# Kernel optimization log

Measured on AMD Instinct MI355X. Metric: run time of the kernel, lower is better.

## Reference

```python
import jax, jax.numpy as jnp
import numpy as np

KERNEL = 25
PAD = (KERNEL - 1) // 2  # 12
LN_EPS = 1e-5
CAP_FACTOR = 2.0
K_VALUE = 2


def _moving_avg(x):
    # x: [B, L, D]; Autoformer moving_avg: replicate-pad ends, avg-pool k=25 stride 1
    front = jnp.repeat(x[:, :1, :], PAD, axis=1)
    end = jnp.repeat(x[:, -1:, :], PAD, axis=1)
    xp = jnp.concatenate([front, x, end], axis=1)            # [B, L+2*PAD, D]
    cs = jnp.cumsum(xp, axis=1)
    cs = jnp.concatenate([jnp.zeros_like(cs[:, :1]), cs], axis=1)
    return (cs[:, KERNEL:] - cs[:, :-KERNEL]) / KERNEL        # [B, L, D]


def _layernorm(h, g, b):
    mu = jnp.mean(h, axis=-1, keepdims=True)
    d = h - mu
    var = jnp.mean(d * d, axis=-1, keepdims=True)
    return d * jax.lax.rsqrt(var + LN_EPS) * g + b


def setup_inputs() -> dict:
    key = jax.random.key(0)
    ks = jax.random.split(key, 6)
    B, L, D, H, E = 32, 512, 512, 1024, 8
    sd_in = 1.0 / np.sqrt(D)
    sd_h = 1.0 / np.sqrt(H)
    return {
        "x": jax.random.normal(ks[0], (B, L, D), jnp.float32),
        "Wt": jax.random.normal(ks[1], (D, H), jnp.float32) * sd_in,
        "bt": jax.random.normal(ks[2], (H,), jnp.float32) * sd_in,
        "gt": jnp.ones((H,), jnp.float32),
        "bet": jnp.zeros((H,), jnp.float32),
        "Ws": jax.random.normal(ks[3], (D, H), jnp.float32) * sd_in,
        "bs": jax.random.normal(ks[4], (H,), jnp.float32) * sd_in,
        "gs": jnp.ones((H,), jnp.float32),
        "bes": jnp.zeros((H,), jnp.float32),
        "W2": jax.random.normal(ks[5], (H, E), jnp.float32) * sd_h,
        "b2": jnp.zeros((E,), jnp.float32),
    }


def reference(x, Wt, bt, gt, bet, Ws, bs, gs, bes, W2, b2):
    # series decomposition: (residual, moving_mean) -> (trend_init, seasonal_init)
    ma = _moving_avg(x)
    trend_init = x - ma          # residual (first return of series_decomp)
    seasonal_init = ma           # moving mean (second return)

    t = _layernorm(trend_init @ Wt + bt, gt, bet)       # [B, L, H]
    s = _layernorm(seasonal_init @ Ws + bs, gs, bes)    # [B, L, H]
    med = jax.nn.relu(t + s)
    logits = med @ W2 + b2                               # [B, L, E]
    gate_scores = jax.nn.softmax(logits, axis=-1)

    B, L, E = gate_scores.shape
    capacity = int(CAP_FACTOR * B)

    _, top_k_indices = jax.lax.top_k(gate_scores, K_VALUE)  # [B, L, K]
    # torch scatter_(1, idx, 1) on 3D: mask[b, idx[b,l,j], j] = 1
    bi = jnp.arange(B)[:, None, None]
    ji = jnp.arange(K_VALUE)[None, None, :]
    mask = jnp.zeros_like(gate_scores).at[bi, top_k_indices, ji].set(1.0)

    masked = gate_scores * mask
    denom = jnp.sum(masked, axis=0, keepdims=True) + 1e-4    # [1, L, E]
    return masked / denom * capacity
```

## Files before the change

kernel.cpp:

```cpp
#include <hip/hip_runtime.h>

#define NB 32
#define NL 512
#define ND 512
#define NH 1024
#define NE 8
#define NROWS (NB * NL)
#define CW 2048
#define SPAD 136

typedef __attribute__((ext_vector_type(8))) short bf16x8;
typedef __attribute__((ext_vector_type(4))) float f32x4;
typedef __attribute__((ext_vector_type(4))) unsigned u32x4;

__device__ __forceinline__ unsigned short f2bf(float f) {
    unsigned u = __float_as_uint(f);
    return (unsigned short)((u + 0x7fffu + ((u >> 16) & 1u)) >> 16);
}
__device__ __forceinline__ float bf2f(unsigned short b) {
    return __uint_as_float(((unsigned)b) << 16);
}
__device__ __forceinline__ unsigned pktr(float a, float b) {
    return __builtin_amdgcn_perm(__float_as_uint(b), __float_as_uint(a), 0x07060302u);
}

__global__ __launch_bounds__(256) void wprep(
    const float* __restrict__ Wt, const float* __restrict__ Ws,
    unsigned* __restrict__ bpack)
{
    __shared__ float tile[64][65];
    int bid = blockIdx.x;
    int mat = bid >> 7, rem = bid & 127;
    int kt0 = (rem >> 4) << 6;
    int nt0 = (rem & 15) << 6;
    const float* W = mat ? Ws : Wt;
    unsigned* Oh = bpack;
    unsigned* Ol = bpack + 524288u;
    int t = threadIdx.x;
    #pragma unroll
    for (int i = 0; i < 16; ++i) {
        int idx = t + 256 * i;
        int k = idx >> 6, n = idx & 63;
        tile[k][n] = W[(size_t)(kt0 + k) * NH + nt0 + n];
    }
    __syncthreads();
    #pragma unroll
    for (int i = 0; i < 8; ++i) {
        int idx = t + 256 * i;
        int jp = idx & 3, lane = (idx >> 2) & 63, kbr = (idx >> 8) & 1, ntr = (idx >> 9) & 3;
        int ncol = ntr * 16 + (lane & 15);
        int kcol = kbr * 32 + ((lane >> 4) << 3) + jp * 2;
        float w0 = tile[kcol][ncol], w1 = tile[kcol + 1][ncol];
        unsigned short h0 = f2bf(w0), h1 = f2bf(w1);
        unsigned short l0 = f2bf(w0 - bf2f(h0)), l1 = f2bf(w1 - bf2f(h1));
        int ntg = mat * 64 + (nt0 >> 4) + ntr;
        int kb = (kt0 >> 5) + kbr;
        unsigned offs = ((unsigned)(ntg * 16 + kb) * 64u + (unsigned)lane) * 4u + jp;
        Oh[offs] = (unsigned)h0 | ((unsigned)h1 << 16);
        Ol[offs] = (unsigned)l0 | ((unsigned)l1 << 16);
    }
}

__global__ __launch_bounds__(512, 4) void gemm_all(
    const float* __restrict__ x, const unsigned* __restrict__ bpack,
    unsigned short* __restrict__ C, unsigned short* __restrict__ Clo)
{
    __shared__ union {
        unsigned short A[2][128][64];
        unsigned short cs[64][264];
    } sm;

    const int tid = threadIdx.x, lane = tid & 63, wave = tid >> 6;
    const int g = lane >> 4, c = lane & 15;

    if (blockIdx.x >= 256) {
        const int wm = wave >> 2, wn = wave & 3;
        const int bid = blockIdx.x - 256;
        const int xcd = bid & 7, idx = bid >> 3;
        const int mi = xcd * 16 + (idx >> 3), ni = idx & 7;
        const int m0 = mi * 128;

        f32x4 acc[4][4];
        #pragma unroll
        for (int nf = 0; nf < 4; ++nf)
            #pragma unroll
            for (int mf = 0; mf < 4; ++mf) acc[nf][mf] = (f32x4){0.f, 0.f, 0.f, 0.f};

        const int srow = tid >> 2, sj = tid & 3;
        const int wcol = (sj * 8) ^ ((srow & 7) << 3);
        const float* xs = x + (size_t)(m0 + srow) * ND + sj * 8;

        auto loadB = [&](int kb2, int nf) -> bf16x8 {
            int nt = ni * 16 + wn * 4 + nf;
            return *(const bf16x8*)(bpack + ((size_t)(nt * 16 + kb2) * 64 + lane) * 4);
        };

        float4 xa = *(const float4*)xs;
        float4 xb = *(const float4*)(xs + 4);
        bf16x8 bc0 = loadB(0, 0), bc1 = loadB(0, 1), bc2 = loadB(0, 2), bc3 = loadB(0, 3);

        int p = 0;
        for (int kb = 0; kb < 16; ++kb) {
            u32x4 u;
            u.x = pktr(xa.x, xa.y); u.y = pktr(xa.z, xa.w);
            u.z = pktr(xb.x, xb.y); u.w = pktr(xb.z, xb.w);
            *(u32x4*)&sm.A[p][srow][wcol] = u;
            __syncthreads();

            bf16x8 bn0, bn1, bn2, bn3;
            if (kb < 15) {
                const float* pn = xs + (kb + 1) * 32;
                xa = *(const float4*)pn;
                xb = *(const float4*)(pn + 4);
                bn0 = loadB(kb + 1, 0); bn1 = loadB(kb + 1, 1);
                bn2 = loadB(kb + 1, 2); bn3 = loadB(kb + 1, 3);
            }

            bf16x8 af[4];
            #pragma unroll
            for (int mf = 0; mf < 4; ++mf) {
                int R = wm * 64 + mf * 16 + c;
                int rcol = (g * 8) ^ ((R & 7) << 3);
                af[mf] = *(const bf16x8*)&sm.A[p][R][rcol];
            }
            #pragma unroll
            for (int mf = 0; mf < 4; ++mf) {
                acc[0][mf] = __builtin_amdgcn_mfma_f32_16x16x32_bf16(af[mf], bc0, acc[0][mf], 0, 0, 0);
                acc[1][mf] = __builtin_amdgcn_mfma_f32_16x16x32_bf16(af[mf], bc1, acc[1][mf], 0, 0, 0);
                acc[2][mf] = __builtin_amdgcn_mfma_f32_16x16x32_bf16(af[mf], bc2, acc[2][mf], 0, 0, 0);
                acc[3][mf] = __builtin_amdgcn_mfma_f32_16x16x32_bf16(af[mf], bc3, acc[3][mf], 0, 0, 0);
            }
            if (kb < 15) { bc0 = bn0; bc1 = bn1; bc2 = bn2; bc3 = bn3; }
            p ^= 1;
        }

        #pragma unroll
        for (int ph = 0; ph < 2; ++ph) {
            __syncthreads();
            if (wm == ph) {
                #pragma unroll
                for (int nf = 0; nf < 4; ++nf)
                    #pragma unroll
                    for (int mf = 0; mf < 4; ++mf)
                        #pragma unroll
                        for (int r = 0; r < 4; ++r)
                            sm.cs[mf * 16 + g * 4 + r][wn * 64 + nf * 16 + c] =
                                (unsigned short)(__float_as_uint(acc[nf][mf][r]) >> 16);
            }
            __syncthreads();
            int row = tid >> 3, ch = tid & 7;
            int grow = m0 + ph * 64 + row;
            if ((grow & 511) >= 32) {
                unsigned short* dst = &C[(size_t)grow * CW + ni * 256 + ch * 32];
                #pragma unroll
                for (int q = 0; q < 4; ++q)
                    *(uint4*)(dst + q * 8) = *(const uint4*)&sm.cs[row][ch * 32 + q * 8];
            }
        }
    } else {
        const int eb = blockIdx.x;
        const int bq = eb >> 3, ni = eb & 7;
        const int m0 = bq * NL;
        const unsigned* Bhi = bpack;
        const unsigned* Blo = bpack + 524288u;

        f32x4 acc[2][2];
        #pragma unroll
        for (int nf = 0; nf < 2; ++nf)
            #pragma unroll
            for (int mf = 0; mf < 2; ++mf) acc[nf][mf] = (f32x4){0.f, 0.f, 0.f, 0.f};

        const float* xr0 = x + (size_t)(m0 + c) * ND + g * 8;
        #pragma unroll 2
        for (int kb = 0; kb < 16; ++kb) {
            bf16x8 ah[2], al[2];
            #pragma unroll
            for (int mf = 0; mf < 2; ++mf) {
                const float* p = xr0 + mf * (16 * ND) + kb * 32;
                float4 a0 = *(const float4*)p;
                float4 a1 = *(const float4*)(p + 4);
                float f[8] = {a0.x, a0.y, a0.z, a0.w, a1.x, a1.y, a1.z, a1.w};
                float lo[8];
                #pragma unroll
                for (int j = 0; j < 8; ++j) {
                    float hif = __uint_as_float(__float_as_uint(f[j]) & 0xFFFF0000u);
                    lo[j] = f[j] - hif;
                }
                u32x4 uh, ul;
                uh.x = pktr(f[0], f[1]); uh.y = pktr(f[2], f[3]);
                uh.z = pktr(f[4], f[5]); uh.w = pktr(f[6], f[7]);
                ul.x = pktr(lo[0], lo[1]); ul.y = pktr(lo[2], lo[3]);
                ul.z = pktr(lo[4], lo[5]); ul.w = pktr(lo[6], lo[7]);
                ah[mf] = __builtin_bit_cast(bf16x8, uh);
                al[mf] = __builtin_bit_cast(bf16x8, ul);
            }
            #pragma unroll
            for (int nf = 0; nf < 2; ++nf) {
                int nt = ni * 16 + wave * 2 + nf;
                size_t bo = ((size_t)(nt * 16 + kb) * 64 + lane) * 4;
                bf16x8 bh = *(const bf16x8*)(Bhi + bo);
                bf16x8 bl = *(const bf16x8*)(Blo + bo);
                #pragma unroll
                for (int mf = 0; mf < 2; ++mf) {
                    acc[nf][mf] = __builtin_amdgcn_mfma_f32_16x16x32_bf16(ah[mf], bh, acc[nf][mf], 0, 0, 0);
                    acc[nf][mf] = __builtin_amdgcn_mfma_f32_16x16x32_bf16(al[mf], bh, acc[nf][mf], 0, 0, 0);
                    acc[nf][mf] = __builtin_amdgcn_mfma_f32_16x16x32_bf16(ah[mf], bl, acc[nf][mf], 0, 0, 0);
                }
            }
        }

        #pragma unroll
        for (int nf = 0; nf < 2; ++nf)
            #pragma unroll
            for (int mf = 0; mf < 2; ++mf)
                #pragma unroll
                for (int r = 0; r < 4; ++r)
                    sm.cs[mf * 16 + g * 4 + r][(wave * 2 + nf) * 16 + c] =
                        (unsigned short)(__float_as_uint(acc[nf][mf][r]) >> 16);
        __syncthreads();
        #pragma unroll
        for (int i = 0; i < 2; ++i) {
            int id = tid + 512 * i;
            int row = id >> 5, cg = id & 31;
            *(uint4*)&C[(size_t)(m0 + row) * CW + ni * 256 + cg * 8] = *(const uint4*)&sm.cs[row][cg * 8];
        }
        __syncthreads();
        #pragma unroll
        for (int nf = 0; nf < 2; ++nf)
            #pragma unroll
            for (int mf = 0; mf < 2; ++mf)
                #pragma unroll
                for (int r = 0; r < 4; ++r) {
                    float v = acc[nf][mf][r];
                    float hif = __uint_as_float(__float_as_uint(v) & 0xFFFF0000u);
                    sm.cs[mf * 16 + g * 4 + r][(wave * 2 + nf) * 16 + c] =
                        (unsigned short)(__float_as_uint(v - hif) >> 16);
                }
        __syncthreads();
        #pragma unroll
        for (int i = 0; i < 2; ++i) {
            int id = tid + 512 * i;
            int row = id >> 5, cg = id & 31;
            if (row < 20)
                *(uint4*)&Clo[((size_t)bq * 20 + row) * CW + ni * 256 + cg * 8] = *(const uint4*)&sm.cs[row][cg * 8];
        }
    }
}

__global__ __launch_bounds__(256) void stats_all(
    const unsigned short* __restrict__ C, const unsigned short* __restrict__ Clo,
    const float* __restrict__ bt, const float* __restrict__ bs,
    float* __restrict__ rowpart, float* __restrict__ exstat)
{
    __shared__ unsigned short stg[88][SPAD];
    const int tid = threadIdx.x;

    if (blockIdx.x < 1024) {
        const int bid = blockIdx.x;
        const int q = bid & 3, lc = (bid >> 2) & 7, b = bid >> 5;
        const int l0 = lc * 64;
        const int cq = tid & 31, rg = tid >> 5;
        const float inv25 = 1.f / 25.f;

        float s[8], qa[8];
        #pragma unroll
        for (int r = 0; r < 8; ++r) { s[r] = 0.f; qa[r] = 0.f; }

        for (int ch = 0; ch < 4; ++ch) {
            int cb = q * 512 + ch * 128;
            __syncthreads();
            for (int i = tid; i < 1408; i += 256) {
                int si = i >> 4, cg = i & 15;
                int gl = l0 - 12 + si;
                gl = gl < 0 ? 0 : (gl > NL - 1 ? NL - 1 : gl);
                *(uint4*)&stg[si][cg * 8] = *(const uint4*)&C[(size_t)(b * NL + gl) * CW + cb + cg * 8];
            }
            __syncthreads();

            float bv[4];
            {
                float4 b4 = q < 2 ? *(const float4*)&bt[cb + cq * 4]
                                  : *(const float4*)&bs[cb - 1024 + cq * 4];
                bv[0] = b4.x; bv[1] = b4.y; bv[2] = b4.z; bv[3] = b4.w;
            }
            float run[4] = {0.f, 0.f, 0.f, 0.f};
            #pragma unroll
            for (int w = 0; w < 25; ++w) {
                ushort4 u = *(const ushort4*)&stg[rg * 8 + w][cq * 4];
                run[0] += bf2f(u.x); run[1] += bf2f(u.y); run[2] += bf2f(u.z); run[3] += bf2f(u.w);
            }
            #pragma unroll
            for (int rr = 0; rr < 8; ++rr) {
                if (rr > 0) {
                    ushort4 un = *(const ushort4*)&stg[rg * 8 + rr + 24][cq * 4];
                    ushort4 uo = *(const ushort4*)&stg[rg * 8 + rr - 1][cq * 4];
                    run[0] += bf2f(un.x) - bf2f(uo.x); run[1] += bf2f(un.y) - bf2f(uo.y);
                    run[2] += bf2f(un.z) - bf2f(uo.z); run[3] += bf2f(un.w) - bf2f(uo.w);
                }
                float pre[4];
                if (q < 2) {
                    ushort4 uc = *(const ushort4*)&stg[rg * 8 + rr + 12][cq * 4];
                    pre[0] = bf2f(uc.x) - run[0] * inv25 + bv[0];
                    pre[1] = bf2f(uc.y) - run[1] * inv25 + bv[1];
                    pre[2] = bf2f(uc.z) - run[2] * inv25 + bv[2];
                    pre[3] = bf2f(uc.w) - run[3] * inv25 + bv[3];
                } else {
                    pre[0] = run[0] * inv25 + bv[0];
                    pre[1] = run[1] * inv25 + bv[1];
                    pre[2] = run[2] * inv25 + bv[2];
                    pre[3] = run[3] * inv25 + bv[3];
                }
                s[rr]  += pre[0] + pre[1] + pre[2] + pre[3];
                qa[rr] += pre[0] * pre[0] + pre[1] * pre[1] + pre[2] * pre[2] + pre[3] * pre[3];
            }
        }

        #pragma unroll
        for (int rr = 0; rr < 8; ++rr)
            #pragma unroll
            for (int o = 1; o < 32; o <<= 1) {
                s[rr]  += __shfl_xor(s[rr], o);
                qa[rr] += __shfl_xor(qa[rr], o);
            }
        if (cq == 0) {
            #pragma unroll
            for (int rr = 0; rr < 8; ++rr) {
                size_t gr = (size_t)b * NL + l0 + rg * 8 + rr;
                rowpart[(gr * 4 + q) * 2 + 0] = s[rr];
                rowpart[(gr * 4 + q) * 2 + 1] = qa[rr];
            }
        }
    } else {
        const int inst = (blockIdx.x - 1024) * 4 + (tid >> 6);
        const int b = inst >> 3, chunk = inst & 7;
        const int t = tid & 63;
        const int c4 = chunk * 256 + t * 4;
        const bool isU = chunk < 4;
        const float inv25 = 1.f / 25.f;

        float bias[4];
        {
            float4 b4 = isU ? *(const float4*)&bt[c4] : *(const float4*)&bs[c4 - 1024];
            bias[0] = b4.x; bias[1] = b4.y; bias[2] = b4.z; bias[3] = b4.w;
        }
        float s[8], q[8];
        #pragma unroll
        for (int r = 0; r < 8; ++r) { s[r] = 0.f; q[r] = 0.f; }

        float cs[4] = {0, 0, 0, 0}, v0[4], keep[8][4];
        #pragma unroll
        for (int j = 0; j < 20; ++j) {
            ushort4 h  = *(const ushort4*)&C[(size_t)(b * NL + j) * CW + c4];
            ushort4 lo = *(const ushort4*)&Clo[((size_t)b * 20 + j) * CW + c4];
            float u[4] = {bf2f(h.x) + bf2f(lo.x), bf2f(h.y) + bf2f(lo.y),
                          bf2f(h.z) + bf2f(lo.z), bf2f(h.w) + bf2f(lo.w)};
            if (j == 0) {
                #pragma unroll
                for (int k = 0; k < 4; ++k) v0[k] = u[k];
            }
            if (j < 8) {
                #pragma unroll
                for (int k = 0; k < 4; ++k) keep[j][k] = u[k];
            }
            #pragma unroll
            for (int k = 0; k < 4; ++k) cs[k] += u[k];
            if (j >= 12) {
                const int l = j - 12;
                const float w0 = (float)(24 - j);
                #pragma unroll
                for (int k = 0; k < 4; ++k) {
                    float ma = (cs[k] + w0 * v0[k]) * inv25;
                    float pre = isU ? (keep[l][k] - ma + bias[k]) : (ma + bias[k]);
                    s[l] += pre;
                    q[l] += pre * pre;
                }
            }
        }
        #pragma unroll
        for (int r = 0; r < 8; ++r)
            #pragma unroll
            for (int o = 1; o < 64; o <<= 1) {
                s[r] += __shfl_xor(s[r], o);
                q[r] += __shfl_xor(q[r], o);
            }
        if (t == 0) {
            #pragma unroll
            for (int r = 0; r < 8; ++r) {
                exstat[(((size_t)b * 8 + chunk) * 8 + r) * 2 + 0] = s[r];
                exstat[(((size_t)b * 8 + chunk) * 8 + r) * 2 + 1] = q[r];
            }
        }
    }
}

__global__ __launch_bounds__(64) void exact_apply(
    const unsigned short* __restrict__ C, const unsigned short* __restrict__ Clo,
    const float* __restrict__ bt, const float* __restrict__ gt, const float* __restrict__ bet,
    const float* __restrict__ bs, const float* __restrict__ gs, const float* __restrict__ bes,
    const float* __restrict__ W2, const float* __restrict__ exstat,
    float* __restrict__ exlg)
{
    const int t = threadIdx.x;
    const int chunk = blockIdx.x & 7, b = blockIdx.x >> 3;
    const int h2 = chunk * 128 + t * 2;
    const float inv25 = 1.f / 25.f;

    float mu_t[8], rs_t[8], mu_s[8], rs_s[8];
    #pragma unroll
    for (int l = 0; l < 8; ++l) {
        float st = 0.f, qt = 0.f, ss = 0.f, qs = 0.f;
        #pragma unroll
        for (int ch = 0; ch < 4; ++ch) {
            st += exstat[(((size_t)b * 8 + ch) * 8 + l) * 2 + 0];
            qt += exstat[(((size_t)b * 8 + ch) * 8 + l) * 2 + 1];
            ss += exstat[(((size_t)b * 8 + 4 + ch) * 8 + l) * 2 + 0];
            qs += exstat[(((size_t)b * 8 + 4 + ch) * 8 + l) * 2 + 1];
        }
        mu_t[l] = st * (1.f / NH);
        rs_t[l] = rsqrtf(qt * (1.f / NH) - mu_t[l] * mu_t[l] + 1e-5f);
        mu_s[l] = ss * (1.f / NH);
        rs_s[l] = rsqrtf(qs * (1.f / NH) - mu_s[l] * mu_s[l] + 1e-5f);
    }

    float btv[2], gtv[2], bev[2], bsv[2], gsv[2], besv[2], w2r[2][NE];
    #pragma unroll
    for (int k = 0; k < 2; ++k) {
        int h = h2 + k;
        btv[k] = bt[h]; gtv[k] = gt[h]; bev[k] = bet[h];
        bsv[k] = bs[h]; gsv[k] = gs[h]; besv[k] = bes[h];
        const float4* wp = (const float4*)&W2[(size_t)h * NE];
        float4 a = wp[0], c2 = wp[1];
        w2r[k][0] = a.x;  w2r[k][1] = a.y;  w2r[k][2] = a.z;  w2r[k][3] = a.w;
        w2r[k][4] = c2.x; w2r[k][5] = c2.y; w2r[k][6] = c2.z; w2r[k][7] = c2.w;
    }

    float csU[2] = {0, 0}, csV[2] = {0, 0}, v0U[2], v0V[2], keepU[8][2];
    float lg[8][NE];
    #pragma unroll
    for (int l = 0; l < 8; ++l)
        #pragma unroll
        for (int e = 0; e < NE; ++e) lg[l][e] = 0.f;

    #pragma unroll
    for (int j = 0; j < 20; ++j) {
        size_t rb = (size_t)(b * NL + j) * CW;
        size_t lb = ((size_t)b * 20 + j) * CW;
        ushort2 hu  = *(const ushort2*)&C[rb + h2];
        ushort2 lu  = *(const ushort2*)&Clo[lb + h2];
        ushort2 hv  = *(const ushort2*)&C[rb + NH + h2];
        ushort2 lv  = *(const ushort2*)&Clo[lb + NH + h2];
        float u[2] = {bf2f(hu.x) + bf2f(lu.x), bf2f(hu.y) + bf2f(lu.y)};
        float v[2] = {bf2f(hv.x) + bf2f(lv.x), bf2f(hv.y) + bf2f(lv.y)};
        if (j == 0) {
            #pragma unroll
            for (int k = 0; k < 2; ++k) { v0U[k] = u[k]; v0V[k] = v[k]; }
        }
        if (j < 8) {
            #pragma unroll
            for (int k = 0; k < 2; ++k) keepU[j][k] = u[k];
        }
        #pragma unroll
        for (int k = 0; k < 2; ++k) { csU[k] += u[k]; csV[k] += v[k]; }
        if (j >= 12) {
            const int l = j - 12;
            const float w0 = (float)(24 - j);
            #pragma unroll
            for (int k = 0; k < 2; ++k) {
                float maU = (csU[k] + w0 * v0U[k]) * inv25;
                float maV = (csV[k] + w0 * v0V[k]) * inv25;
                float tn = ((keepU[l][k] - maU + btv[k]) - mu_t[l]) * rs_t[l] * gtv[k] + bev[k];
                float sn = ((maV + bsv[k]) - mu_s[l]) * rs_s[l] * gsv[k] + besv[k];
                float m = tn + sn; m = m > 0.f ? m : 0.f;
                #pragma unroll
                for (int e = 0; e < NE; ++e) lg[l][e] = fmaf(m, w2r[k][e], lg[l][e]);
            }
        }
    }
    #pragma unroll
    for (int l = 0; l < 8; ++l)
        #pragma unroll
        for (int e = 0; e < NE; ++e)
            #pragma unroll
            for (int o = 1; o < 64; o <<= 1)
                lg[l][e] += __shfl_xor(lg[l][e], o);
    if (t == 0) {
        #pragma unroll
        for (int l = 0; l < 8; ++l)
            #pragma unroll
            for (int e = 0; e < NE; ++e)
                exlg[(((size_t)b * 8 + chunk) * 8 + l) * NE + e] = lg[l][e];
    }
}

__global__ __launch_bounds__(256) void apply_k(
    const unsigned short* __restrict__ C,
    const float* __restrict__ bt, const float* __restrict__ gt, const float* __restrict__ bet,
    const float* __restrict__ bs, const float* __restrict__ gs, const float* __restrict__ bes,
    const float* __restrict__ W2, const float* __restrict__ rowpart,
    float* __restrict__ lgpart)
{
    __shared__ unsigned short stgU[88][SPAD];
    __shared__ unsigned short stgV[88][SPAD];
    __shared__ float4 rowstat[64];

    const int tid = threadIdx.x;
    const int bid = blockIdx.x;
    const int q = bid & 3, lc = (bid >> 2) & 7, b = bid >> 5;
    const int l0 = lc * 64;
    const int cq = tid & 31, rg = tid >> 5;
    const float inv25 = 1.f / 25.f;

    if (tid < 64) {
        size_t gr = (size_t)b * NL + l0 + tid;
        const float* p = &rowpart[gr * 8];
        float st = p[0] + p[2], qt = p[1] + p[3];
        float ss = p[4] + p[6], qs = p[5] + p[7];
        float mut = st * (1.f / NH), mus = ss * (1.f / NH);
        float vt = qt * (1.f / NH) - mut * mut;
        float vs = qs * (1.f / NH) - mus * mus;
        rowstat[tid] = make_float4(mut, rsqrtf(vt + 1e-5f), mus, rsqrtf(vs + 1e-5f));
    }

    float lgp[8][NE];
    #pragma unroll
    for (int r = 0; r < 8; ++r)
        #pragma unroll
        for (int e = 0; e < NE; ++e) lgp[r][e] = 0.f;

    for (int ch = 0; ch < 2; ++ch) {
        int hb = q * 256 + ch * 128;
        __syncthreads();
        for (int i = tid; i < 1408; i += 256) {
            int si = i >> 4, cg = i & 15;
            int gl = l0 - 12 + si;
            gl = gl < 0 ? 0 : (gl > NL - 1 ? NL - 1 : gl);
            size_t rb = (size_t)(b * NL + gl) * CW;
            *(uint4*)&stgU[si][cg * 8] = *(const uint4*)&C[rb + hb + cg * 8];
            *(uint4*)&stgV[si][cg * 8] = *(const uint4*)&C[rb + NH + hb + cg * 8];
        }
        __syncthreads();

        int col = hb + cq * 4;
        float4 btv = *(const float4*)&bt[col],  gtv = *(const float4*)&gt[col];
        float4 bev = *(const float4*)&bet[col], bsv = *(const float4*)&bs[col];
        float4 gsv = *(const float4*)&gs[col],  besv = *(const float4*)&bes[col];
        float btr[4] = {btv.x, btv.y, btv.z, btv.w};
        float gtr[4] = {gtv.x, gtv.y, gtv.z, gtv.w};
        float ber[4] = {bev.x, bev.y, bev.z, bev.w};
        float bsr[4] = {bsv.x, bsv.y, bsv.z, bsv.w};
        float gsr[4] = {gsv.x, gsv.y, gsv.z, gsv.w};
        float besr[4] = {besv.x, besv.y, besv.z, besv.w};
        float w2r[4][NE];
        #pragma unroll
        for (int j = 0; j < 4; ++j) {
            const float4* wp = (const float4*)&W2[(size_t)(col + j) * NE];
            float4 a = wp[0], c2 = wp[1];
            w2r[j][0] = a.x;  w2r[j][1] = a.y;  w2r[j][2] = a.z;  w2r[j][3] = a.w;
            w2r[j][4] = c2.x; w2r[j][5] = c2.y; w2r[j][6] = c2.z; w2r[j][7] = c2.w;
        }

        float runU[4] = {0.f, 0.f, 0.f, 0.f}, runV[4] = {0.f, 0.f, 0.f, 0.f};
        #pragma unroll
        for (int w = 0; w < 25; ++w) {
            ushort4 u = *(const ushort4*)&stgU[rg * 8 + w][cq * 4];
            ushort4 v = *(const ushort4*)&stgV[rg * 8 + w][cq * 4];
            runU[0] += bf2f(u.x); runU[1] += bf2f(u.y); runU[2] += bf2f(u.z); runU[3] += bf2f(u.w);
            runV[0] += bf2f(v.x); runV[1] += bf2f(v.y); runV[2] += bf2f(v.z); runV[3] += bf2f(v.w);
        }
        #pragma unroll
        for (int rr = 0; rr < 8; ++rr) {
            if (rr > 0) {
                ushort4 un = *(const ushort4*)&stgU[rg * 8 + rr + 24][cq * 4];
                ushort4 uo = *(const ushort4*)&stgU[rg * 8 + rr - 1][cq * 4];
                ushort4 vn = *(const ushort4*)&stgV[rg * 8 + rr + 24][cq * 4];
                ushort4 vo = *(const ushort4*)&stgV[rg * 8 + rr - 1][cq * 4];
                runU[0] += bf2f(un.x) - bf2f(uo.x); runU[1] += bf2f(un.y) - bf2f(uo.y);
                runU[2] += bf2f(un.z) - bf2f(uo.z); runU[3] += bf2f(un.w) - bf2f(uo.w);
                runV[0] += bf2f(vn.x) - bf2f(vo.x); runV[1] += bf2f(vn.y) - bf2f(vo.y);
                runV[2] += bf2f(vn.z) - bf2f(vo.z); runV[3] += bf2f(vn.w) - bf2f(vo.w);
            }
            float4 rs = rowstat[rg * 8 + rr];
            ushort4 uc = *(const ushort4*)&stgU[rg * 8 + rr + 12][cq * 4];
            float cen[4] = {bf2f(uc.x), bf2f(uc.y), bf2f(uc.z), bf2f(uc.w)};
            float med[4];
            #pragma unroll
            for (int j = 0; j < 4; ++j) {
                float tn = ((cen[j] - runU[j] * inv25 + btr[j]) - rs.x) * rs.y * gtr[j] + ber[j];
                float sn = ((runV[j] * inv25 + bsr[j]) - rs.z) * rs.w * gsr[j] + besr[j];
                float m = tn + sn;
                med[j] = m > 0.f ? m : 0.f;
            }
            #pragma unroll
            for (int e = 0; e < NE; ++e)
                lgp[rr][e] = fmaf(med[0], w2r[0][e], fmaf(med[1], w2r[1][e],
                             fmaf(med[2], w2r[2][e], fmaf(med[3], w2r[3][e], lgp[rr][e]))));
        }
    }

    #pragma unroll
    for (int rr = 0; rr < 8; ++rr)
        #pragma unroll
        for (int e = 0; e < NE; ++e)
            #pragma unroll
            for (int o = 1; o < 32; o <<= 1)
                lgp[rr][e] += __shfl_xor(lgp[rr][e], o);
    if (cq == 0) {
        #pragma unroll
        for (int rr = 0; rr < 8; ++rr) {
            size_t gr = (size_t)b * NL + l0 + rg * 8 + rr;
            #pragma unroll
            for (int e = 0; e < NE; ++e)
                lgpart[(gr * 4 + q) * NE + e] = lgp[rr][e];
        }
    }
}

__global__ __launch_bounds__(256) void final_all(
    const float* __restrict__ lgpart, const float* __restrict__ exlg,
    const float* __restrict__ b2,
    unsigned* __restrict__ mb, float* __restrict__ gates)
{
    const int t = threadIdx.x;
    if (blockIdx.x < 64) {
        int row = blockIdx.x * 256 + t;
        int b = row >> 9, l = row & (NL - 1);
        float lg[NE];
        #pragma unroll
        for (int e = 0; e < NE; ++e) lg[e] = b2[e];
        #pragma unroll
        for (int qq = 0; qq < 4; ++qq)
            #pragma unroll
            for (int e = 0; e < NE; ++e)
                lg[e] += lgpart[((size_t)row * 4 + qq) * NE + e];
        int i0 = 0;
        #pragma unroll
        for (int e = 1; e < NE; ++e) if (lg[e] > lg[i0]) i0 = e;
        int i1 = i0 == 0 ? 1 : 0;
        #pragma unroll
        for (int e = 0; e < NE; ++e) if (e != i0 && lg[e] > lg[i1]) i1 = e;
        unsigned m = (l < 8) ? 0u : ((1u << i0) | (1u << (8 + i1)));
        #pragma unroll
        for (int o = 1; o < 64; o <<= 1) m |= __shfl_xor(m, o);
        if ((t & 63) == 0) {
            atomicOr(&mb[2 * b + 0], m & 0xffu);
            atomicOr(&mb[2 * b + 1], m >> 8);
        }
    } else {
        const int b = t >> 3, l = t & 7;
        float lg[NE];
        #pragma unroll
        for (int e = 0; e < NE; ++e) lg[e] = b2[e];
        #pragma unroll
        for (int ch = 0; ch < 8; ++ch)
            #pragma unroll
            for (int e = 0; e < NE; ++e)
                lg[e] += exlg[(((size_t)b * 8 + ch) * 8 + l) * NE + e];
        float mx = lg[0];
        #pragma unroll
        for (int e = 1; e < NE; ++e) mx = lg[e] > mx ? lg[e] : mx;
        float p[NE]; float sum = 0.f;
        #pragma unroll
        for (int e = 0; e < NE; ++e) { p[e] = expf(lg[e] - mx); sum += p[e]; }
        float inv = 1.f / sum;
        #pragma unroll
        for (int e = 0; e < NE; ++e)
            gates[((size_t)b * 8 + l) * NE + e] = p[e] * inv;
        int i0 = 0;
        #pragma unroll
        for (int e = 1; e < NE; ++e) if (lg[e] > lg[i0]) i0 = e;
        int i1 = i0 == 0 ? 1 : 0;
        #pragma unroll
        for (int e = 0; e < NE; ++e) if (e != i0 && lg[e] > lg[i1]) i1 = e;
        unsigned m = (1u << i0) | (1u << (8 + i1));
        m |= __shfl_xor(m, 1); m |= __shfl_xor(m, 2); m |= __shfl_xor(m, 4);
        if (l == 0) {
            atomicOr(&mb[2 * b + 0], m & 0xffu);
            atomicOr(&mb[2 * b + 1], m >> 8);
        }
    }
}

__global__ void finalize_k(const unsigned* __restrict__ mb,
                           const float* __restrict__ gates,
                           float* __restrict__ out)
{
    int t = threadIdx.x;
    if (t >= 16) return;
    int l = t >> 1, e = t & 1;
    float m[NB];
    float sum = 0.f;
    #pragma unroll
    for (int bb = 0; bb < NB; ++bb) {
        float gvv = gates[((size_t)bb * 8 + l) * NE + e];
        float on  = ((mb[2 * bb + e] >> l) & 1u) ? 1.f : 0.f;
        m[bb] = gvv * on;
        sum += m[bb];
    }
    float scale = 64.f / (sum + 1e-4f);
    #pragma unroll
    for (int bb = 0; bb < NB; ++bb)
        out[(size_t)bb * (NL * NE) + l * NE + e] = m[bb] * scale;
}

extern "C" void kernel_launch(void* const* d_in, const int* in_sizes, int n_in,
                              void* d_out, int out_size, void* d_ws, size_t ws_size,
                              hipStream_t stream) {
    const float* x   = (const float*)d_in[0];
    const float* Wt  = (const float*)d_in[1];
    const float* bt  = (const float*)d_in[2];
    const float* gt  = (const float*)d_in[3];
    const float* bet = (const float*)d_in[4];
    const float* Ws  = (const float*)d_in[5];
    const float* bs  = (const float*)d_in[6];
    const float* gs  = (const float*)d_in[7];
    const float* bes = (const float*)d_in[8];
    const float* W2  = (const float*)d_in[9];
    const float* b2  = (const float*)d_in[10];
    float* out = (float*)d_out;

    char* wsb = (char*)d_ws;
    unsigned*       mbp     = (unsigned*)wsb;
    float*          gates   = (float*)(wsb + 256);
    unsigned*       bpack   = (unsigned*)(wsb + 4096);
    float*          rowpart = (float*)(wsb + 4096);
    float*          lgpart  = (float*)(wsb + 4096 + 524288);
    float*          exstat  = (float*)(wsb + 4096 + 524288 + 2097152);
    float*          exlg    = (float*)(wsb + 4096 + 524288 + 2097152 + 16384);
    unsigned short* C       = (unsigned short*)(wsb + 4096 + 4194304);
    unsigned short* Clo     = (unsigned short*)(wsb + 4096 + 4194304 + (size_t)NROWS * CW * 2);

    hipMemsetAsync(d_out, 0, sizeof(float) * NB * NL * NE, stream);
    hipMemsetAsync(mbp, 0, 256, stream);

    wprep<<<256, 256, 0, stream>>>(Wt, Ws, bpack);
    gemm_all<<<1280, 512, 0, stream>>>(x, bpack, C, Clo);
    stats_all<<<1088, 256, 0, stream>>>(C, Clo, bt, bs, rowpart, exstat);
    exact_apply<<<256, 64, 0, stream>>>(C, Clo, bt, gt, bet, bs, gs, bes, W2, exstat, exlg);
    apply_k<<<1024, 256, 0, stream>>>(C, bt, gt, bet, bs, gs, bes, W2, rowpart, lgpart);
    final_all<<<65, 256, 0, stream>>>(lgpart, exlg, b2, mbp, gates);
    finalize_k<<<1, 64, 0, stream>>>(mbp, gates, out);
}
```

Before: 174.0 us.

## Shrink GEMM blocks to 256 threads with 64-row M tiles and padded LDS

The main GEMM path now uses 256-thread blocks with 64-row M tiles instead of 512-thread blocks with 128-row tiles. The grid grows from 1280 to 2304 blocks, the A tile in LDS is row-padded (stride 40) instead of XOR-swizzled, and the first barrier moves after the prefetch loads. The exact-path blocks take 4 N-fragments per wave to match the smaller block. The aim is higher occupancy and simpler LDS addressing and epilogue. The cost is less reuse of B per block, so B is refetched twice as often, and the padded layout may cause bank conflicts.

```diff
diff --git a/kernel.cpp b/kernel.cpp
--- a/kernel.cpp
+++ b/kernel.cpp
@@ -61,12 +61,12 @@
     }
 }
 
-__global__ __launch_bounds__(512, 4) void gemm_all(
+__global__ __launch_bounds__(256, 4) void gemm_all(
     const float* __restrict__ x, const unsigned* __restrict__ bpack,
     unsigned short* __restrict__ C, unsigned short* __restrict__ Clo)
 {
     __shared__ union {
-        unsigned short A[2][128][64];
+        unsigned short A[2][64][40];
         unsigned short cs[64][264];
     } sm;
 
@@ -74,11 +74,10 @@
     const int g = lane >> 4, c = lane & 15;
 
     if (blockIdx.x >= 256) {
-        const int wm = wave >> 2, wn = wave & 3;
         const int bid = blockIdx.x - 256;
         const int xcd = bid & 7, idx = bid >> 3;
-        const int mi = xcd * 16 + (idx >> 3), ni = idx & 7;
-        const int m0 = mi * 128;
+        const int mi = xcd * 32 + (idx >> 3), ni = idx & 7;
+        const int m0 = mi * 64;
 
         f32x4 acc[4][4];
         #pragma unroll
@@ -87,11 +86,10 @@
             for (int mf = 0; mf < 4; ++mf) acc[nf][mf] = (f32x4){0.f, 0.f, 0.f, 0.f};
 
         const int srow = tid >> 2, sj = tid & 3;
-        const int wcol = (sj * 8) ^ ((srow & 7) << 3);
         const float* xs = x + (size_t)(m0 + srow) * ND + sj * 8;
 
         auto loadB = [&](int kb2, int nf) -> bf16x8 {
-            int nt = ni * 16 + wn * 4 + nf;
+            int nt = ni * 16 + wave * 4 + nf;
             return *(const bf16x8*)(bpack + ((size_t)(nt * 16 + kb2) * 64 + lane) * 4);
         };
 
@@ -99,14 +97,12 @@
         float4 xb = *(const float4*)(xs + 4);
         bf16x8 bc0 = loadB(0, 0), bc1 = loadB(0, 1), bc2 = loadB(0, 2), bc3 = loadB(0, 3);
 
-        int p = 0;
         for (int kb = 0; kb < 16; ++kb) {
+            const int p = kb & 1;
             u32x4 u;
             u.x = pktr(xa.x, xa.y); u.y = pktr(xa.z, xa.w);
             u.z = pktr(xb.x, xb.y); u.w = pktr(xb.z, xb.w);
-            *(u32x4*)&sm.A[p][srow][wcol] = u;
-            __syncthreads();
-
+            *(u32x4*)&sm.A[p][srow][sj * 8] = u;
             bf16x8 bn0, bn1, bn2, bn3;
             if (kb < 15) {
                 const float* pn = xs + (kb + 1) * 32;
@@ -115,14 +111,12 @@
                 bn0 = loadB(kb + 1, 0); bn1 = loadB(kb + 1, 1);
                 bn2 = loadB(kb + 1, 2); bn3 = loadB(kb + 1, 3);
             }
+            __syncthreads();
 
             bf16x8 af[4];
             #pragma unroll
-            for (int mf = 0; mf < 4; ++mf) {
-                int R = wm * 64 + mf * 16 + c;
-                int rcol = (g * 8) ^ ((R & 7) << 3);
-                af[mf] = *(const bf16x8*)&sm.A[p][R][rcol];
-            }
+            for (int mf = 0; mf < 4; ++mf)
+                af[mf] = *(const bf16x8*)&sm.A[p][mf * 16 + c][g * 8];
             #pragma unroll
             for (int mf = 0; mf < 4; ++mf) {
                 acc[0][mf] = __builtin_amdgcn_mfma_f32_16x16x32_bf16(af[mf], bc0, acc[0][mf], 0, 0, 0);
@@ -131,31 +125,25 @@
                 acc[3][mf] = __builtin_amdgcn_mfma_f32_16x16x32_bf16(af[mf], bc3, acc[3][mf], 0, 0, 0);
             }
             if (kb < 15) { bc0 = bn0; bc1 = bn1; bc2 = bn2; bc3 = bn3; }
-            p ^= 1;
-        }
-
-        #pragma unroll
-        for (int ph = 0; ph < 2; ++ph) {
-            __syncthreads();
-            if (wm == ph) {
-                #pragma unroll
-                for (int nf = 0; nf < 4; ++nf)
-                    #pragma unroll
-                    for (int mf = 0; mf < 4; ++mf)
-                        #pragma unroll
-                        for (int r = 0; r < 4; ++r)
-                            sm.cs[mf * 16 + g * 4 + r][wn * 64 + nf * 16 + c] =
-                                (unsigned short)(__float_as_uint(acc[nf][mf][r]) >> 16);
-            }
-            __syncthreads();
-            int row = tid >> 3, ch = tid & 7;
-            int grow = m0 + ph * 64 + row;
-            if ((grow & 511) >= 32) {
-                unsigned short* dst = &C[(size_t)grow * CW + ni * 256 + ch * 32];
-                #pragma unroll
-                for (int q = 0; q < 4; ++q)
-                    *(uint4*)(dst + q * 8) = *(const uint4*)&sm.cs[row][ch * 32 + q * 8];
-            }
+        }
+
+        __syncthreads();
+        #pragma unroll
+        for (int nf = 0; nf < 4; ++nf)
+            #pragma unroll
+            for (int mf = 0; mf < 4; ++mf)
+                #pragma unroll
+                for (int r = 0; r < 4; ++r)
+                    sm.cs[mf * 16 + g * 4 + r][wave * 64 + nf * 16 + c] =
+                        (unsigned short)(__float_as_uint(acc[nf][mf][r]) >> 16);
+        __syncthreads();
+        #pragma unroll
+        for (int i = 0; i < 8; ++i) {
+            int idx2 = tid + 256 * i;
+            int row = idx2 >> 5, cg = idx2 & 31;
+            int grow = m0 + row;
+            if ((grow & 511) >= 32)
+                *(uint4*)&C[(size_t)grow * CW + ni * 256 + cg * 8] = *(const uint4*)&sm.cs[row][cg * 8];
         }
     } else {
         const int eb = blockIdx.x;
@@ -164,9 +152,9 @@
         const unsigned* Bhi = bpack;
         const unsigned* Blo = bpack + 524288u;
 
-        f32x4 acc[2][2];
-        #pragma unroll
-        for (int nf = 0; nf < 2; ++nf)
+        f32x4 acc[4][2];
+        #pragma unroll
+        for (int nf = 0; nf < 4; ++nf)
             #pragma unroll
             for (int mf = 0; mf < 2; ++mf) acc[nf][mf] = (f32x4){0.f, 0.f, 0.f, 0.f};
 
@@ -195,8 +183,8 @@
                 al[mf] = __builtin_bit_cast(bf16x8, ul);
             }
             #pragma unroll
-            for (int nf = 0; nf < 2; ++nf) {
-                int nt = ni * 16 + wave * 2 + nf;
+            for (int nf = 0; nf < 4; ++nf) {
+                int nt = ni * 16 + wave * 4 + nf;
                 size_t bo = ((size_t)(nt * 16 + kb) * 64 + lane) * 4;
                 bf16x8 bh = *(const bf16x8*)(Bhi + bo);
                 bf16x8 bl = *(const bf16x8*)(Blo + bo);
@@ -210,37 +198,37 @@
         }
 
         #pragma unroll
-        for (int nf = 0; nf < 2; ++nf)
+        for (int nf = 0; nf < 4; ++nf)
             #pragma unroll
             for (int mf = 0; mf < 2; ++mf)
                 #pragma unroll
                 for (int r = 0; r < 4; ++r)
-                    sm.cs[mf * 16 + g * 4 + r][(wave * 2 + nf) * 16 + c] =
+                    sm.cs[mf * 16 + g * 4 + r][wave * 64 + nf * 16 + c] =
                         (unsigned short)(__float_as_uint(acc[nf][mf][r]) >> 16);
         __syncthreads();
         #pragma unroll
-        for (int i = 0; i < 2; ++i) {
-            int id = tid + 512 * i;
-            int row = id >> 5, cg = id & 31;
+        for (int i = 0; i < 4; ++i) {
+            int idx2 = tid + 256 * i;
+            int row = idx2 >> 5, cg = idx2 & 31;
             *(uint4*)&C[(size_t)(m0 + row) * CW + ni * 256 + cg * 8] = *(const uint4*)&sm.cs[row][cg * 8];
         }
         __syncthreads();
         #pragma unroll
-        for (int nf = 0; nf < 2; ++nf)
+        for (int nf = 0; nf < 4; ++nf)
             #pragma unroll
             for (int mf = 0; mf < 2; ++mf)
                 #pragma unroll
                 for (int r = 0; r < 4; ++r) {
                     float v = acc[nf][mf][r];
                     float hif = __uint_as_float(__float_as_uint(v) & 0xFFFF0000u);
-                    sm.cs[mf * 16 + g * 4 + r][(wave * 2 + nf) * 16 + c] =
+                    sm.cs[mf * 16 + g * 4 + r][wave * 64 + nf * 16 + c] =
                         (unsigned short)(__float_as_uint(v - hif) >> 16);
                 }
         __syncthreads();
         #pragma unroll
-        for (int i = 0; i < 2; ++i) {
-            int id = tid + 512 * i;
-            int row = id >> 5, cg = id & 31;
+        for (int i = 0; i < 3; ++i) {
+            int idx2 = tid + 256 * i;
+            int row = idx2 >> 5, cg = idx2 & 31;
             if (row < 20)
                 *(uint4*)&Clo[((size_t)bq * 20 + row) * CW + ni * 256 + cg * 8] = *(const uint4*)&sm.cs[row][cg * 8];
         }
@@ -347,7 +335,7 @@
         #pragma unroll
         for (int r = 0; r < 8; ++r) { s[r] = 0.f; q[r] = 0.f; }
 
-        float cs[4] = {0, 0, 0, 0}, v0[4], keep[8][4];
+        float cs2[4] = {0, 0, 0, 0}, v0[4], keep[8][4];
         #pragma unroll
         for (int j = 0; j < 20; ++j) {
             ushort4 h  = *(const ushort4*)&C[(size_t)(b * NL + j) * CW + c4];
@@ -363,13 +351,13 @@
                 for (int k = 0; k < 4; ++k) keep[j][k] = u[k];
             }
             #pragma unroll
-            for (int k = 0; k < 4; ++k) cs[k] += u[k];
+            for (int k = 0; k < 4; ++k) cs2[k] += u[k];
             if (j >= 12) {
                 const int l = j - 12;
                 const float w0 = (float)(24 - j);
                 #pragma unroll
                 for (int k = 0; k < 4; ++k) {
-                    float ma = (cs[k] + w0 * v0[k]) * inv25;
+                    float ma = (cs2[k] + w0 * v0[k]) * inv25;
                     float pre = isU ? (keep[l][k] - ma + bias[k]) : (ma + bias[k]);
                     s[l] += pre;
                     q[l] += pre * pre;
@@ -733,7 +721,7 @@
     hipMemsetAsync(mbp, 0, 256, stream);
 
     wprep<<<256, 256, 0, stream>>>(Wt, Ws, bpack);
-    gemm_all<<<1280, 512, 0, stream>>>(x, bpack, C, Clo);
+    gemm_all<<<2304, 256, 0, stream>>>(x, bpack, C, Clo);
     stats_all<<<1088, 256, 0, stream>>>(C, Clo, bt, bs, rowpart, exstat);
     exact_apply<<<256, 64, 0, stream>>>(C, Clo, bt, gt, bet, bs, gs, bes, W2, exstat, exlg);
     apply_k<<<1024, 256, 0, stream>>>(C, bt, gt, bet, bs, gs, bes, W2, rowpart, lgpart);
```

Result: faster. 158.6 us (-8.9%).
